# Kernel tuning notes

Measured on AMD Instinct MI355X. Metric: run time of the kernel, lower is better.

## Reference

```python
import jax, jax.numpy as jnp
import numpy as np

DIM = 32      # state dim (enc_shape[0])
LDIM = 256    # latent dim (enc_shape[-1])
N_AUX = LDIM // 2
AUX_H = 128   # aux hidden
ENC_H = 256   # encoder hidden
T = 64        # n_shifts
N = 1024      # batch
DT = 0.01


def setup_inputs() -> dict:
    key = jax.random.key(0)
    ks = jax.random.split(key, 13)
    def w(k, shape, fan):
        return jax.random.normal(k, shape, jnp.float32) / np.sqrt(fan).astype(np.float32)
    return {
        "xs": jax.random.normal(ks[0], (N, T, DIM), jnp.float32),
        # encoder MLP: dim -> 256 -> 256 -> ldim (last layer has no bias)
        "enc_W1": w(ks[1], (DIM, ENC_H), DIM), "enc_b1": w(ks[2], (ENC_H,), ENC_H),
        "enc_W2": w(ks[3], (ENC_H, ENC_H), ENC_H), "enc_b2": w(ks[4], (ENC_H,), ENC_H),
        "enc_W3": w(ks[5], (ENC_H, LDIM), ENC_H),
        # n_aux independent aux MLPs: dim -> 128 -> 128 -> 2 (last no bias), stacked
        "aux_W1": w(ks[6], (N_AUX, DIM, AUX_H), DIM), "aux_b1": w(ks[7], (N_AUX, AUX_H), AUX_H),
        "aux_W2": w(ks[8], (N_AUX, AUX_H, AUX_H), AUX_H), "aux_b2": w(ks[9], (N_AUX, AUX_H), AUX_H),
        "aux_W3": w(ks[10], (N_AUX, AUX_H, 2), AUX_H),
        # C: Linear(ldim, dim, bias=False); stored as [ldim, dim] so x_next = y @ C_W
        "C_W": w(ks[11], (LDIM, DIM), LDIM),
    }


def reference(xs, enc_W1, enc_b1, enc_W2, enc_b2, enc_W3,
              aux_W1, aux_b1, aux_W2, aux_b2, aux_W3, C_W):
    x0 = xs[:, 0, :]                                    # [N, dim]
    # all n_aux tiny MLPs batched via einsum (instead of python loop)
    h = jax.nn.relu(jnp.einsum('nd,kdh->nkh', x0, aux_W1) + aux_b1)
    h = jax.nn.relu(jnp.einsum('nkh,khg->nkg', h, aux_W2) + aux_b2)
    aux = jnp.einsum('nkh,kho->nko', h, aux_W3)          # [N, n_aux, 2] -> (mu, omega)
    scale = jnp.exp(aux[..., 0] * DT)
    cos = jnp.cos(aux[..., 1] * DT) * scale              # [N, n_aux]
    sin = jnp.sin(aux[..., 1] * DT) * scale

    # encoder over all n_shifts timesteps
    e = jax.nn.relu(xs @ enc_W1 + enc_b1)
    e = jax.nn.relu(e @ enc_W2 + enc_b2)
    e = e @ enc_W3                                       # [N, T, ldim]
    y = jnp.concatenate([xs, e], axis=-1)                # [N, T, dim+ldim]

    # Koopman recurrence. The original builds a block-diagonal [ldim, ldim]
    # matrix of 2x2 rotation-scaling blocks (block k acts on latent pair
    # (2k, 2k+1)) and applies it as a row-vector bmm: out = y_row @ K with
    # K_block = [[cos, sin], [-sin, cos]]. We apply the blocks directly.
    y0 = e[:, 0, :].reshape(N, N_AUX, 2)
    def step(carry, _):
        y1, y2 = carry[..., 0], carry[..., 1]
        yn = jnp.stack([y1 * cos - y2 * sin, y1 * sin + y2 * cos], axis=-1)
        return yn, yn
    _, ys = jax.lax.scan(step, y0, None, length=T - 1)   # [T-1, N, n_aux, 2]
    ys = jnp.moveaxis(ys, 0, 1).reshape(N, T - 1, LDIM)  # [N, T-1, ldim]

    y_lat = jnp.concatenate([e[:, :1, :], ys], axis=1)          # [N, T, ldim]
    x_pred = jnp.concatenate([xs[:, :1, :], ys @ C_W], axis=1)  # [N, T, dim]
    y_pred = jnp.concatenate([x_pred, y_lat], axis=-1)          # [N, T, dim+ldim]
    return y, y_pred
```

## Files before the change

### kernel.cpp

```cpp
#include <hip/hip_runtime.h>
#include <math.h>

#define N_SEQ 1024
#define T_SEQ 64
#define DIMX  32
#define LDIM  256
#define NAUX  128
#define AUXH  128
#define ENCH  256
#define OUTC  288
#define DT    0.01f

typedef short bf16x8 __attribute__((ext_vector_type(8)));
typedef float f32x4  __attribute__((ext_vector_type(4)));

__device__ __forceinline__ unsigned short f2bf(float f) {
    unsigned u = __builtin_bit_cast(unsigned, f);
    unsigned r = u + 0x7fffu + ((u >> 16) & 1u);
    return (unsigned short)(r >> 16);
}
__device__ __forceinline__ float bf2f(unsigned short h) {
    unsigned u = ((unsigned)h) << 16;
    return __builtin_bit_cast(float, u);
}
__device__ __forceinline__ f32x4 mfma16(bf16x8 a, bf16x8 b, f32x4 c) {
    return __builtin_amdgcn_mfma_f32_16x16x32_bf16(a, b, c, 0, 0, 0);
}

#define CV_ENC   139264
#define PREP_CONV_BLOCKS 576
__global__ __launch_bounds__(256) void prep_kernel(
    const float* __restrict__ eW1, const float* __restrict__ eW2,
    const float* __restrict__ eW3, const float* __restrict__ C_W,
    const float* __restrict__ aW1, const float* __restrict__ aW2,
    unsigned short* __restrict__ encw, float* __restrict__ cwt,
    unsigned short* __restrict__ a1h, unsigned short* __restrict__ a1l,
    unsigned short* __restrict__ a2h, unsigned short* __restrict__ a2l)
{
    __shared__ float tile[32][33];
    const int b   = blockIdx.x;
    const int tid = threadIdx.x;

    if (b < PREP_CONV_BLOCKS) {
        const int idx = b * 256 + tid;
        if (idx < 8192) {
            int c = idx >> 5, k = idx & 31;
            encw[idx] = f2bf(eW1[k * ENCH + c]);
        } else if (idx < 8192 + 65536) {
            int t = idx - 8192; int c = t >> 8, k = t & 255;
            encw[idx] = f2bf(eW2[k * ENCH + c]);
        } else if (idx < CV_ENC) {
            int t = idx - (8192 + 65536); int c = t >> 8, k = t & 255;
            encw[idx] = f2bf(eW3[k * LDIM + c]);
        } else if (idx < CV_ENC + 8192) {
            int t = idx - CV_ENC; int d = t >> 8, l = t & 255;
            cwt[t] = C_W[l * DIMX + d];
        }
        return;
    }

    const int bb0 = b - PREP_CONV_BLOCKS;
    const float* src; unsigned short *dh, *dl; int R, j0, r0;
    if (bb0 < 512) {
        int k = bb0 >> 2; j0 = (bb0 & 3) * 32; r0 = 0; R = 32;
        src = aW1 + (size_t)k * 4096;
        dh = a1h + (size_t)k * 4096; dl = a1l + (size_t)k * 4096;
    } else {
        int bb = bb0 - 512;
        int k = bb >> 4; j0 = ((bb >> 2) & 3) * 32; r0 = (bb & 3) * 32; R = 128;
        src = aW2 + (size_t)k * 16384;
        dh = a2h + (size_t)k * 16384; dl = a2l + (size_t)k * 16384;
    }

    for (int i = tid; i < 1024; i += 256) {
        int rr = i >> 5, jj = i & 31;
        tile[rr][jj] = src[(r0 + rr) * 128 + j0 + jj];
    }
    __syncthreads();
    for (int i = tid; i < 1024; i += 256) {
        int jj = i >> 5, rr = i & 31;
        float w = tile[rr][jj];
        unsigned short hi = f2bf(w);
        int off = (j0 + jj) * R + r0 + rr;
        dh[off] = hi;
        dl[off] = f2bf(w - bf2f(hi));
    }
}

__global__ __launch_bounds__(256) void auxm_kernel(
    const float* __restrict__ xs,
    const unsigned short* __restrict__ W1h, const unsigned short* __restrict__ W1l,
    const float* __restrict__ b1,
    const unsigned short* __restrict__ W2h, const unsigned short* __restrict__ W2l,
    const float* __restrict__ b2,
    const float* __restrict__ W3,
    float* __restrict__ a_ws, float* __restrict__ th_ws)
{
    const int k   = blockIdx.x >> 4;
    const int n0  = (blockIdx.x & 15) << 6;
    const int tid = threadIdx.x;
    const int wv  = tid >> 6;
    const int ln  = tid & 63;
    const int lr  = ln & 15;
    const int g   = ln >> 4;
    const int cb  = wv * 32;

    __shared__ unsigned short x0h[64][40];
    __shared__ unsigned short x0l[64][40];
    __shared__ unsigned short h1h[64][136];
    __shared__ unsigned short h1l[64][136];
    __shared__ float          p3[256];

    for (int i = tid; i < 512; i += 256) {
        int r = i >> 3, qd = i & 7;
        float4 v = *(const float4*)&xs[(size_t)(n0 + r) * (T_SEQ * DIMX) + qd * 4];
        short4 hs, ls;
        float vv[4] = {v.x, v.y, v.z, v.w};
        short* hp = (short*)&hs; short* lp = (short*)&ls;
        #pragma unroll
        for (int u = 0; u < 4; ++u) {
            unsigned short hi = f2bf(vv[u]);
            hp[u] = (short)hi;
            lp[u] = (short)f2bf(vv[u] - bf2f(hi));
        }
        *(short4*)&x0h[r][qd * 4] = hs;
        *(short4*)&x0l[r][qd * 4] = ls;
    }
    __syncthreads();

    {
        const unsigned short* W1hk = W1h + (size_t)k * 4096;
        const unsigned short* W1lk = W1l + (size_t)k * 4096;
        bf16x8 bh[2], bl[2];
        #pragma unroll
        for (int ct = 0; ct < 2; ++ct) {
            int off = (cb + ct * 16 + lr) * 32 + g * 8;
            bh[ct] = *(const bf16x8*)&W1hk[off];
            bl[ct] = *(const bf16x8*)&W1lk[off];
        }
        f32x4 acc[4][2];
        #pragma unroll
        for (int rt = 0; rt < 4; ++rt) {
            bf16x8 ah = *(const bf16x8*)&x0h[rt * 16 + lr][g * 8];
            bf16x8 al = *(const bf16x8*)&x0l[rt * 16 + lr][g * 8];
            #pragma unroll
            for (int ct = 0; ct < 2; ++ct) {
                f32x4 z = {0.f, 0.f, 0.f, 0.f};
                z = mfma16(ah, bl[ct], z);
                z = mfma16(al, bh[ct], z);
                acc[rt][ct] = mfma16(ah, bh[ct], z);
            }
        }
        #pragma unroll
        for (int ct = 0; ct < 2; ++ct) {
            const int col = cb + ct * 16 + lr;
            const float bb = b1[k * 128 + col];
            #pragma unroll
            for (int rt = 0; rt < 4; ++rt)
                #pragma unroll
                for (int i = 0; i < 4; ++i) {
                    float h = fmaxf(acc[rt][ct][i] + bb, 0.f);
                    unsigned short hi = f2bf(h);
                    int row = rt * 16 + g * 4 + i;
                    h1h[row][col] = hi;
                    h1l[row][col] = f2bf(h - bf2f(hi));
                }
        }
    }
    __syncthreads();

    {
        const unsigned short* W2hk = W2h + (size_t)k * 16384;
        const unsigned short* W2lk = W2l + (size_t)k * 16384;
        f32x4 acc[4][2];
        #pragma unroll
        for (int rt = 0; rt < 4; ++rt)
            #pragma unroll
            for (int ct = 0; ct < 2; ++ct) acc[rt][ct] = (f32x4){0.f,0.f,0.f,0.f};

        #pragma unroll
        for (int kk = 0; kk < 4; ++kk) {
            bf16x8 bh[2], bl[2], ah[4], al[4];
            #pragma unroll
            for (int ct = 0; ct < 2; ++ct) {
                int off = (cb + ct * 16 + lr) * 128 + kk * 32 + g * 8;
                bh[ct] = *(const bf16x8*)&W2hk[off];
                bl[ct] = *(const bf16x8*)&W2lk[off];
            }
            #pragma unroll
            for (int rt = 0; rt < 4; ++rt) {
                ah[rt] = *(const bf16x8*)&h1h[rt * 16 + lr][kk * 32 + g * 8];
                al[rt] = *(const bf16x8*)&h1l[rt * 16 + lr][kk * 32 + g * 8];
            }
            #pragma unroll
            for (int rt = 0; rt < 4; ++rt)
                #pragma unroll
                for (int ct = 0; ct < 2; ++ct) {
                    f32x4 z = acc[rt][ct];
                    z = mfma16(ah[rt], bl[ct], z);
                    z = mfma16(al[rt], bh[ct], z);
                    acc[rt][ct] = mfma16(ah[rt], bh[ct], z);
                }
        }
        __syncthreads();
        #pragma unroll
        for (int ct = 0; ct < 2; ++ct) {
            const int col = cb + ct * 16 + lr;
            const float bb = b2[k * 128 + col];
            #pragma unroll
            for (int rt = 0; rt < 4; ++rt)
                #pragma unroll
                for (int i = 0; i < 4; ++i) {
                    float h = fmaxf(acc[rt][ct][i] + bb, 0.f);
                    unsigned short hi = f2bf(h);
                    int row = rt * 16 + g * 4 + i;
                    h1h[row][col] = hi;
                    h1l[row][col] = f2bf(h - bf2f(hi));
                }
        }
    }
    __syncthreads();

    {
        const int hh = tid >> 7, r = tid & 127, n = r >> 1, o = r & 1;
        const float* W3k = W3 + (size_t)k * (AUXH * 2);
        float s = 0.f;
        #pragma unroll
        for (int h8 = hh * 64; h8 < hh * 64 + 64; h8 += 8) {
            bf16x8 vh = *(const bf16x8*)&h1h[n][h8];
            bf16x8 vl = *(const bf16x8*)&h1l[n][h8];
            #pragma unroll
            for (int u = 0; u < 8; ++u) {
                float hv = bf2f((unsigned short)vh[u]) + bf2f((unsigned short)vl[u]);
                s += hv * W3k[(h8 + u) * 2 + o];
            }
        }
        p3[tid] = s;
    }
    __syncthreads();
    if (tid < 128) {
        const int n = tid >> 1, o = tid & 1;
        float v = (p3[tid] + p3[tid + 128]) * DT;
        float* dst = o ? th_ws : a_ws;
        dst[(size_t)(n0 + n) * NAUX + k] = v;
    }
}

__global__ __launch_bounds__(256) void encm_kernel(
    const float* __restrict__ xs,
    const unsigned short* __restrict__ W1T, const float* __restrict__ b1,
    const unsigned short* __restrict__ W2T, const float* __restrict__ b2,
    const unsigned short* __restrict__ W3T,
    float* __restrict__ y)
{
    __shared__ float          Xf[64 * 36];
    __shared__ unsigned short Hs[64 * 264];

    const int tid = threadIdx.x;
    const int wv  = tid >> 6;
    const int ln  = tid & 63;
    const int lr  = ln & 15;
    const int g   = ln >> 4;
    const int cb  = wv * 64;
    const size_t row0 = (size_t)blockIdx.x * 64;

    {
        const float4* src = (const float4*)(xs + row0 * DIMX);
        for (int i = tid; i < 512; i += 256) {
            int r = i >> 3, q = i & 7;
            *(float4*)&Xf[r * 36 + q * 4] = src[i];
        }
    }
    __syncthreads();

    {
        f32x4 acc[4][4];
        bf16x8 bfr[4], afr[4];
        #pragma unroll
        for (int ct = 0; ct < 4; ++ct)
            bfr[ct] = *(const bf16x8*)&W1T[(cb + ct * 16 + lr) * 32 + g * 8];
        #pragma unroll
        for (int rt = 0; rt < 4; ++rt) {
            const float* xp = &Xf[(rt * 16 + lr) * 36 + g * 8];
            float4 u = *(const float4*)xp;
            float4 v = *(const float4*)(xp + 4);
            bf16x8 t;
            t[0]=(short)f2bf(u.x); t[1]=(short)f2bf(u.y); t[2]=(short)f2bf(u.z); t[3]=(short)f2bf(u.w);
            t[4]=(short)f2bf(v.x); t[5]=(short)f2bf(v.y); t[6]=(short)f2bf(v.z); t[7]=(short)f2bf(v.w);
            afr[rt] = t;
        }
        #pragma unroll
        for (int rt = 0; rt < 4; ++rt)
            #pragma unroll
            for (int ct = 0; ct < 4; ++ct) {
                f32x4 z = {0.f, 0.f, 0.f, 0.f};
                acc[rt][ct] = mfma16(afr[rt], bfr[ct], z);
            }
        #pragma unroll
        for (int ct = 0; ct < 4; ++ct) {
            const float bb = b1[cb + ct * 16 + lr];
            #pragma unroll
            for (int rt = 0; rt < 4; ++rt)
                #pragma unroll
                for (int i = 0; i < 4; ++i) {
                    float h = fmaxf(acc[rt][ct][i] + bb, 0.f);
                    Hs[(rt * 16 + g * 4 + i) * 264 + cb + ct * 16 + lr] = f2bf(h);
                }
        }
    }
    __syncthreads();

    int wrow[4], hoff[4];
    #pragma unroll
    for (int ct = 0; ct < 4; ++ct) wrow[ct] = (cb + ct * 16 + lr) * 256 + g * 8;
    #pragma unroll
    for (int rt = 0; rt < 4; ++rt) hoff[rt] = (rt * 16 + lr) * 264 + g * 8;

    {
        f32x4 acc[4][4];
        #pragma unroll
        for (int rt = 0; rt < 4; ++rt)
            #pragma unroll
            for (int ct = 0; ct < 4; ++ct) acc[rt][ct] = (f32x4){0.f,0.f,0.f,0.f};
        #pragma unroll 2
        for (int kk = 0; kk < 8; ++kk) {
            bf16x8 bfr[4], afr[4];
            #pragma unroll
            for (int ct = 0; ct < 4; ++ct)
                bfr[ct] = *(const bf16x8*)&W2T[wrow[ct] + kk * 32];
            #pragma unroll
            for (int rt = 0; rt < 4; ++rt)
                afr[rt] = *(const bf16x8*)&Hs[hoff[rt] + kk * 32];
            #pragma unroll
            for (int rt = 0; rt < 4; ++rt)
                #pragma unroll
                for (int ct = 0; ct < 4; ++ct)
                    acc[rt][ct] = mfma16(afr[rt], bfr[ct], acc[rt][ct]);
        }
        __syncthreads();
        #pragma unroll
        for (int ct = 0; ct < 4; ++ct) {
            const float bb = b2[cb + ct * 16 + lr];
            #pragma unroll
            for (int rt = 0; rt < 4; ++rt)
                #pragma unroll
                for (int i = 0; i < 4; ++i) {
                    float h = fmaxf(acc[rt][ct][i] + bb, 0.f);
                    Hs[(rt * 16 + g * 4 + i) * 264 + cb + ct * 16 + lr] = f2bf(h);
                }
        }
    }
    __syncthreads();

    {
        f32x4 acc[4][4];
        #pragma unroll
        for (int rt = 0; rt < 4; ++rt)
            #pragma unroll
            for (int ct = 0; ct < 4; ++ct) acc[rt][ct] = (f32x4){0.f,0.f,0.f,0.f};
        #pragma unroll 2
        for (int kk = 0; kk < 8; ++kk) {
            bf16x8 bfr[4], afr[4];
            #pragma unroll
            for (int ct = 0; ct < 4; ++ct)
                bfr[ct] = *(const bf16x8*)&W3T[wrow[ct] + kk * 32];
            #pragma unroll
            for (int rt = 0; rt < 4; ++rt)
                afr[rt] = *(const bf16x8*)&Hs[hoff[rt] + kk * 32];
            #pragma unroll
            for (int rt = 0; rt < 4; ++rt)
                #pragma unroll
                for (int ct = 0; ct < 4; ++ct)
                    acc[rt][ct] = mfma16(afr[rt], bfr[ct], acc[rt][ct]);
        }
        #pragma unroll
        for (int ct = 0; ct < 4; ++ct) {
            const int c3 = cb + ct * 16 + lr;
            #pragma unroll
            for (int rt = 0; rt < 4; ++rt)
                #pragma unroll
                for (int i = 0; i < 4; ++i)
                    y[(row0 + rt * 16 + g * 4 + i) * OUTC + DIMX + c3] = acc[rt][ct][i];
        }
    }

    for (int i = tid; i < 512; i += 256) {
        int r = i >> 3, q = i & 7;
        *(float4*)&y[(row0 + r) * OUTC + q * 4] = *(const float4*)&Xf[r * 36 + q * 4];
    }
}

__global__ __launch_bounds__(256) void enc0_kernel(
    const float* __restrict__ xs,
    const float* __restrict__ W1, const float* __restrict__ b1,
    const float* __restrict__ W2, const float* __restrict__ b2,
    const float* __restrict__ W3,
    float* __restrict__ y)
{
    __shared__ float Xs[4 * 32];
    __shared__ float Hsf[4 * 256];
    const int tid = threadIdx.x;
    const int c   = tid;
    const int n0  = blockIdx.x * 4;

    if (tid < 32) {
        int r = tid >> 3, q = tid & 7;
        *(float4*)&Xs[r * 32 + q * 4] =
            *(const float4*)&xs[(size_t)(n0 + r) * (T_SEQ * DIMX) + q * 4];
    }
    __syncthreads();

    float acc[4];
    {
        float w[32];
        #pragma unroll
        for (int d = 0; d < 32; ++d) w[d] = W1[d * ENCH + c];
        const float bb = b1[c];
        #pragma unroll
        for (int r = 0; r < 4; ++r) {
            float a = bb;
            #pragma unroll
            for (int d4 = 0; d4 < 8; ++d4) {
                float4 xv = *(const float4*)&Xs[r * 32 + d4 * 4];
                a += xv.x * w[d4*4] + xv.y * w[d4*4+1] + xv.z * w[d4*4+2] + xv.w * w[d4*4+3];
            }
            acc[r] = a;
        }
        #pragma unroll
        for (int r = 0; r < 4; ++r) Hsf[r * 256 + c] = fmaxf(acc[r], 0.f);
    }
    __syncthreads();
    {
        const float bb = b2[c];
        #pragma unroll
        for (int r = 0; r < 4; ++r) acc[r] = bb;
        for (int hc = 0; hc < 8; ++hc) {
            float w[32];
            #pragma unroll
            for (int i = 0; i < 32; ++i) w[i] = W2[(hc * 32 + i) * ENCH + c];
            #pragma unroll
            for (int r = 0; r < 4; ++r) {
                float a = acc[r];
                #pragma unroll
                for (int h4 = 0; h4 < 8; ++h4) {
                    float4 hv = *(const float4*)&Hsf[r * 256 + hc * 32 + h4 * 4];
                    a += hv.x * w[h4*4] + hv.y * w[h4*4+1] + hv.z * w[h4*4+2] + hv.w * w[h4*4+3];
                }
                acc[r] = a;
            }
        }
        __syncthreads();
        #pragma unroll
        for (int r = 0; r < 4; ++r) Hsf[r * 256 + c] = fmaxf(acc[r], 0.f);
    }
    __syncthreads();
    {
        #pragma unroll
        for (int r = 0; r < 4; ++r) acc[r] = 0.f;
        for (int hc = 0; hc < 8; ++hc) {
            float w[32];
            #pragma unroll
            for (int i = 0; i < 32; ++i) w[i] = W3[(hc * 32 + i) * LDIM + c];
            #pragma unroll
            for (int r = 0; r < 4; ++r) {
                float a = acc[r];
                #pragma unroll
                for (int h4 = 0; h4 < 8; ++h4) {
                    float4 hv = *(const float4*)&Hsf[r * 256 + hc * 32 + h4 * 4];
                    a += hv.x * w[h4*4] + hv.y * w[h4*4+1] + hv.z * w[h4*4+2] + hv.w * w[h4*4+3];
                }
                acc[r] = a;
            }
        }
    }
    #pragma unroll
    for (int r = 0; r < 4; ++r)
        y[((size_t)(n0 + r) * T_SEQ) * OUTC + DIMX + c] = acc[r];
}

__global__ __launch_bounds__(256) void scan3_kernel(
    const float* __restrict__ xs,
    const float* __restrict__ a_ws, const float* __restrict__ th_ws,
    const float* __restrict__ cwt,
    const float* __restrict__ y,
    float* __restrict__ yp)
{
    __shared__ float ys_lds[16][256];

    const int n = blockIdx.x >> 2;
    const int q = blockIdx.x & 3;
    const int e = threadIdx.x;
    const int k = e >> 1;

    const float* yrow0 = y + (size_t)n * T_SEQ * OUTC + DIMX;
    float2 y0 = *(const float2*)&yrow0[e & ~1];
    const float a  = a_ws [n * NAUX + k];
    const float th = th_ws[n * NAUX + k];

    const float m = expf(a);
    float ss, cc; sincosf(th, &ss, &cc);
    const float zr = m * cc, zi = m * ss;

    float pr = zr, pi = zi;
    #pragma unroll
    for (int s2 = 0; s2 < 4; ++s2) {
        float nr = pr * pr - pi * pi;
        pi = 2.f * pr * pi; pr = nr;
    }
    float wr = 1.f, wi = 0.f;
    for (int j = 0; j < q; ++j) {
        float nr = wr * pr - wi * pi;
        wi = wr * pi + wi * pr; wr = nr;
    }

    const bool imag = e & 1;
    float* ypn = yp + (size_t)n * T_SEQ * OUTC;

    #pragma unroll 4
    for (int tl = 0; tl < 16; ++tl) {
        const int t = q * 16 + tl;
        float val = imag ? (y0.x * wi + y0.y * wr)
                         : (y0.x * wr - y0.y * wi);
        ypn[(size_t)t * OUTC + DIMX + e] = val;
        ys_lds[tl][(e + ((tl >> 1) & 7) * 4) & 255] = val;
        float nwr = wr * zr - wi * zi;
        wi = wr * zi + wi * zr;
        wr = nwr;
    }
    __syncthreads();

    const int d  = e >> 3;
    const int tg = e & 7;
    const float* cwd = cwt + d * 256;
    const int rot = tg * 4;

    #pragma unroll
    for (int s = 0; s < 2; ++s) {
        const int tl = tg * 2 + s;
        const int t  = q * 16 + tl;
        float o;
        if (t == 0) {
            o = xs[(size_t)n * T_SEQ * DIMX + d];
        } else {
            float sum = 0.f;
            #pragma unroll 8
            for (int l = 0; l < 256; l += 4) {
                const int c0 = (l + rot) & 255;
                float4 yv = *(const float4*)&ys_lds[tl][c0];
                float4 wv = *(const float4*)&cwd[l];
                sum += yv.x * wv.x + yv.y * wv.y + yv.z * wv.z + yv.w * wv.w;
            }
            o = sum;
        }
        ypn[(size_t)t * OUTC + d] = o;
    }
}

extern "C" void kernel_launch(void* const* d_in, const int* in_sizes, int n_in,
                              void* d_out, int out_size, void* d_ws, size_t ws_size,
                              hipStream_t stream)
{
    const float* xs   = (const float*)d_in[0];
    const float* eW1  = (const float*)d_in[1];
    const float* eb1  = (const float*)d_in[2];
    const float* eW2  = (const float*)d_in[3];
    const float* eb2  = (const float*)d_in[4];
    const float* eW3  = (const float*)d_in[5];
    const float* aW1  = (const float*)d_in[6];
    const float* ab1  = (const float*)d_in[7];
    const float* aW2  = (const float*)d_in[8];
    const float* ab2  = (const float*)d_in[9];
    const float* aW3  = (const float*)d_in[10];
    const float* C_W  = (const float*)d_in[11];

    float* y  = (float*)d_out;
    float* yp = y + (size_t)N_SEQ * T_SEQ * OUTC;

    float* a_ws  = (float*)d_ws;
    float* th_ws = a_ws + (size_t)N_SEQ * NAUX;
    unsigned short* encw = (unsigned short*)(th_ws + (size_t)N_SEQ * NAUX);
    unsigned short* W1T = encw;
    unsigned short* W2T = encw + 8192;
    unsigned short* W3T = encw + 8192 + 65536;
    unsigned short* a1h = encw + CV_ENC;
    unsigned short* a1l = a1h + 524288;
    unsigned short* a2h = a1l + 524288;
    unsigned short* a2l = a2h + 2097152;
    float* cwt = (float*)(a2l + 2097152);

    prep_kernel<<<PREP_CONV_BLOCKS + 2560, 256, 0, stream>>>(
        eW1, eW2, eW3, C_W, aW1, aW2, encw, cwt, a1h, a1l, a2h, a2l);
    auxm_kernel <<<128 * 16, 256, 0, stream>>>(
        xs, a1h, a1l, ab1, a2h, a2l, ab2, aW3, a_ws, th_ws);
    encm_kernel <<<N_SEQ * T_SEQ / 64, 256, 0, stream>>>(xs, W1T, eb1, W2T, eb2, W3T, y);
    enc0_kernel <<<N_SEQ / 4, 256, 0, stream>>>(xs, eW1, eb1, eW2, eb2, eW3, y);
    scan3_kernel<<<N_SEQ * 4, 256, 0, stream>>>(xs, a_ws, th_ws, cwt, y, yp);
}
```

Measured before the change: 190.9 us.

## Merge aux and encoder kernels into one launch, fold enc0 into prep

The aux-MLP and encoder-MFMA kernels are combined into a single main_kernel whose block index picks the role, so both workloads share one launch and can overlap on the GPU. The fp32 t=0 encoder pass is moved into extra blocks of the prep kernel, and the encoder's output write now skips row t=0 so that row keeps the fp32 result. The scan's C projection computes two timesteps together so each weight load is reused. This cuts two launches and the idle tails between them, in exchange for a larger shared-memory footprint and more branching per block.

```diff
diff --git a/kernel.cpp b/kernel.cpp
--- a/kernel.cpp
+++ b/kernel.cpp
@@ -13,13 +13,14 @@
 
 typedef short bf16x8 __attribute__((ext_vector_type(8)));
 typedef float f32x4  __attribute__((ext_vector_type(4)));
-
-__device__ __forceinline__ unsigned short f2bf(float f) {
+typedef unsigned short ush;
+
+__device__ __forceinline__ ush f2bf(float f) {
     unsigned u = __builtin_bit_cast(unsigned, f);
     unsigned r = u + 0x7fffu + ((u >> 16) & 1u);
-    return (unsigned short)(r >> 16);
+    return (ush)(r >> 16);
 }
-__device__ __forceinline__ float bf2f(unsigned short h) {
+__device__ __forceinline__ float bf2f(ush h) {
     unsigned u = ((unsigned)h) << 16;
     return __builtin_bit_cast(float, u);
 }
@@ -29,15 +30,20 @@
 
 #define CV_ENC   139264
 #define PREP_CONV_BLOCKS 576
+#define PREP_TR_BLOCKS   2560
+#define PREP_ENC0_BLOCKS 256
 __global__ __launch_bounds__(256) void prep_kernel(
-    const float* __restrict__ eW1, const float* __restrict__ eW2,
+    const float* __restrict__ eW1, const float* __restrict__ eb1,
+    const float* __restrict__ eW2, const float* __restrict__ eb2,
     const float* __restrict__ eW3, const float* __restrict__ C_W,
     const float* __restrict__ aW1, const float* __restrict__ aW2,
-    unsigned short* __restrict__ encw, float* __restrict__ cwt,
-    unsigned short* __restrict__ a1h, unsigned short* __restrict__ a1l,
-    unsigned short* __restrict__ a2h, unsigned short* __restrict__ a2l)
+    const float* __restrict__ xs,
+    ush* __restrict__ encw, float* __restrict__ cwt,
+    ush* __restrict__ a1h, ush* __restrict__ a1l,
+    ush* __restrict__ a2h, ush* __restrict__ a2l,
+    float* __restrict__ y)
 {
-    __shared__ float tile[32][33];
+    __shared__ float psm[1152];
     const int b   = blockIdx.x;
     const int tid = threadIdx.x;
 
@@ -59,423 +65,433 @@
         return;
     }
 
-    const int bb0 = b - PREP_CONV_BLOCKS;
-    const float* src; unsigned short *dh, *dl; int R, j0, r0;
-    if (bb0 < 512) {
-        int k = bb0 >> 2; j0 = (bb0 & 3) * 32; r0 = 0; R = 32;
-        src = aW1 + (size_t)k * 4096;
-        dh = a1h + (size_t)k * 4096; dl = a1l + (size_t)k * 4096;
-    } else {
-        int bb = bb0 - 512;
-        int k = bb >> 4; j0 = ((bb >> 2) & 3) * 32; r0 = (bb & 3) * 32; R = 128;
-        src = aW2 + (size_t)k * 16384;
-        dh = a2h + (size_t)k * 16384; dl = a2l + (size_t)k * 16384;
-    }
-
-    for (int i = tid; i < 1024; i += 256) {
-        int rr = i >> 5, jj = i & 31;
-        tile[rr][jj] = src[(r0 + rr) * 128 + j0 + jj];
-    }
-    __syncthreads();
-    for (int i = tid; i < 1024; i += 256) {
-        int jj = i >> 5, rr = i & 31;
-        float w = tile[rr][jj];
-        unsigned short hi = f2bf(w);
-        int off = (j0 + jj) * R + r0 + rr;
-        dh[off] = hi;
-        dl[off] = f2bf(w - bf2f(hi));
+    if (b < PREP_CONV_BLOCKS + PREP_TR_BLOCKS) {
+        float (*tile)[33] = (float(*)[33])psm;
+        const int bb0 = b - PREP_CONV_BLOCKS;
+        const float* src; ush *dh, *dl; int R, j0, r0;
+        if (bb0 < 512) {
+            int k = bb0 >> 2; j0 = (bb0 & 3) * 32; r0 = 0; R = 32;
+            src = aW1 + (size_t)k * 4096;
+            dh = a1h + (size_t)k * 4096; dl = a1l + (size_t)k * 4096;
+        } else {
+            int bb = bb0 - 512;
+            int k = bb >> 4; j0 = ((bb >> 2) & 3) * 32; r0 = (bb & 3) * 32; R = 128;
+            src = aW2 + (size_t)k * 16384;
+            dh = a2h + (size_t)k * 16384; dl = a2l + (size_t)k * 16384;
+        }
+        for (int i = tid; i < 1024; i += 256) {
+            int rr = i >> 5, jj = i & 31;
+            tile[rr][jj] = src[(r0 + rr) * 128 + j0 + jj];
+        }
+        __syncthreads();
+        for (int i = tid; i < 1024; i += 256) {
+            int jj = i >> 5, rr = i & 31;
+            float w = tile[rr][jj];
+            ush hi = f2bf(w);
+            int off = (j0 + jj) * R + r0 + rr;
+            dh[off] = hi;
+            dl[off] = f2bf(w - bf2f(hi));
+        }
+        return;
+    }
+
+    {
+        float* Xs  = psm;
+        float* Hsf = psm + 128;
+        const int c  = tid;
+        const int n0 = (b - PREP_CONV_BLOCKS - PREP_TR_BLOCKS) * 4;
+
+        if (tid < 32) {
+            int r = tid >> 3, q = tid & 7;
+            *(float4*)&Xs[r * 32 + q * 4] =
+                *(const float4*)&xs[(size_t)(n0 + r) * (T_SEQ * DIMX) + q * 4];
+        }
+        __syncthreads();
+
+        float acc[4];
+        {
+            float w[32];
+            #pragma unroll
+            for (int d = 0; d < 32; ++d) w[d] = eW1[d * ENCH + c];
+            const float bb = eb1[c];
+            #pragma unroll
+            for (int r = 0; r < 4; ++r) {
+                float a = bb;
+                #pragma unroll
+                for (int d4 = 0; d4 < 8; ++d4) {
+                    float4 xv = *(const float4*)&Xs[r * 32 + d4 * 4];
+                    a += xv.x * w[d4*4] + xv.y * w[d4*4+1] + xv.z * w[d4*4+2] + xv.w * w[d4*4+3];
+                }
+                acc[r] = a;
+            }
+            #pragma unroll
+            for (int r = 0; r < 4; ++r) Hsf[r * 256 + c] = fmaxf(acc[r], 0.f);
+        }
+        __syncthreads();
+        {
+            const float bb = eb2[c];
+            #pragma unroll
+            for (int r = 0; r < 4; ++r) acc[r] = bb;
+            for (int hc = 0; hc < 8; ++hc) {
+                float w[32];
+                #pragma unroll
+                for (int i = 0; i < 32; ++i) w[i] = eW2[(hc * 32 + i) * ENCH + c];
+                #pragma unroll
+                for (int r = 0; r < 4; ++r) {
+                    float a = acc[r];
+                    #pragma unroll
+                    for (int h4 = 0; h4 < 8; ++h4) {
+                        float4 hv = *(const float4*)&Hsf[r * 256 + hc * 32 + h4 * 4];
+                        a += hv.x * w[h4*4] + hv.y * w[h4*4+1] + hv.z * w[h4*4+2] + hv.w * w[h4*4+3];
+                    }
+                    acc[r] = a;
+                }
+            }
+            __syncthreads();
+            #pragma unroll
+            for (int r = 0; r < 4; ++r) Hsf[r * 256 + c] = fmaxf(acc[r], 0.f);
+        }
+        __syncthreads();
+        {
+            #pragma unroll
+            for (int r = 0; r < 4; ++r) acc[r] = 0.f;
+            for (int hc = 0; hc < 8; ++hc) {
+                float w[32];
+                #pragma unroll
+                for (int i = 0; i < 32; ++i) w[i] = eW3[(hc * 32 + i) * LDIM + c];
+                #pragma unroll
+                for (int r = 0; r < 4; ++r) {
+                    float a = acc[r];
+                    #pragma unroll
+                    for (int h4 = 0; h4 < 8; ++h4) {
+                        float4 hv = *(const float4*)&Hsf[r * 256 + hc * 32 + h4 * 4];
+                        a += hv.x * w[h4*4] + hv.y * w[h4*4+1] + hv.z * w[h4*4+2] + hv.w * w[h4*4+3];
+                    }
+                    acc[r] = a;
+                }
+            }
+        }
+        #pragma unroll
+        for (int r = 0; r < 4; ++r)
+            y[((size_t)(n0 + r) * T_SEQ) * OUTC + DIMX + c] = acc[r];
     }
 }
 
-__global__ __launch_bounds__(256) void auxm_kernel(
+__global__ __launch_bounds__(256) void main_kernel(
     const float* __restrict__ xs,
-    const unsigned short* __restrict__ W1h, const unsigned short* __restrict__ W1l,
-    const float* __restrict__ b1,
-    const unsigned short* __restrict__ W2h, const unsigned short* __restrict__ W2l,
-    const float* __restrict__ b2,
-    const float* __restrict__ W3,
-    float* __restrict__ a_ws, float* __restrict__ th_ws)
+    const ush* __restrict__ W1h, const ush* __restrict__ W1l,
+    const float* __restrict__ ab1,
+    const ush* __restrict__ W2h, const ush* __restrict__ W2l,
+    const float* __restrict__ ab2,
+    const float* __restrict__ aW3,
+    float* __restrict__ a_ws, float* __restrict__ th_ws,
+    const ush* __restrict__ W1T, const float* __restrict__ eb1,
+    const ush* __restrict__ W2T, const float* __restrict__ eb2,
+    const ush* __restrict__ W3T,
+    float* __restrict__ y)
 {
-    const int k   = blockIdx.x >> 4;
-    const int n0  = (blockIdx.x & 15) << 6;
+    __shared__ __align__(16) char smem[46080];
     const int tid = threadIdx.x;
     const int wv  = tid >> 6;
     const int ln  = tid & 63;
     const int lr  = ln & 15;
     const int g   = ln >> 4;
-    const int cb  = wv * 32;
-
-    __shared__ unsigned short x0h[64][40];
-    __shared__ unsigned short x0l[64][40];
-    __shared__ unsigned short h1h[64][136];
-    __shared__ unsigned short h1l[64][136];
-    __shared__ float          p3[256];
-
-    for (int i = tid; i < 512; i += 256) {
-        int r = i >> 3, qd = i & 7;
-        float4 v = *(const float4*)&xs[(size_t)(n0 + r) * (T_SEQ * DIMX) + qd * 4];
-        short4 hs, ls;
-        float vv[4] = {v.x, v.y, v.z, v.w};
-        short* hp = (short*)&hs; short* lp = (short*)&ls;
+
+    if (blockIdx.x < 2048) {
+        ush (*x0h)[40]  = (ush(*)[40]) (smem);
+        ush (*x0l)[40]  = (ush(*)[40]) (smem + 5120);
+        ush (*h1h)[136] = (ush(*)[136])(smem + 10240);
+        ush (*h1l)[136] = (ush(*)[136])(smem + 27648);
+        float* p3       = (float*)     (smem + 45056);
+
+        const int k   = blockIdx.x >> 4;
+        const int n0  = (blockIdx.x & 15) << 6;
+        const int cb  = wv * 32;
+
+        for (int i = tid; i < 512; i += 256) {
+            int r = i >> 3, qd = i & 7;
+            float4 v = *(const float4*)&xs[(size_t)(n0 + r) * (T_SEQ * DIMX) + qd * 4];
+            short4 hs, ls;
+            float vv[4] = {v.x, v.y, v.z, v.w};
+            short* hp = (short*)&hs; short* lp = (short*)&ls;
+            #pragma unroll
+            for (int u = 0; u < 4; ++u) {
+                ush hi = f2bf(vv[u]);
+                hp[u] = (short)hi;
+                lp[u] = (short)f2bf(vv[u] - bf2f(hi));
+            }
+            *(short4*)&x0h[r][qd * 4] = hs;
+            *(short4*)&x0l[r][qd * 4] = ls;
+        }
+        __syncthreads();
+
+        {
+            const ush* W1hk = W1h + (size_t)k * 4096;
+            const ush* W1lk = W1l + (size_t)k * 4096;
+            bf16x8 bh[2], bl[2];
+            #pragma unroll
+            for (int ct = 0; ct < 2; ++ct) {
+                int off = (cb + ct * 16 + lr) * 32 + g * 8;
+                bh[ct] = *(const bf16x8*)&W1hk[off];
+                bl[ct] = *(const bf16x8*)&W1lk[off];
+            }
+            f32x4 acc[4][2];
+            #pragma unroll
+            for (int rt = 0; rt < 4; ++rt) {
+                bf16x8 ah = *(const bf16x8*)&x0h[rt * 16 + lr][g * 8];
+                bf16x8 al = *(const bf16x8*)&x0l[rt * 16 + lr][g * 8];
+                #pragma unroll
+                for (int ct = 0; ct < 2; ++ct) {
+                    f32x4 z = {0.f, 0.f, 0.f, 0.f};
+                    z = mfma16(ah, bl[ct], z);
+                    z = mfma16(al, bh[ct], z);
+                    acc[rt][ct] = mfma16(ah, bh[ct], z);
+                }
+            }
+            #pragma unroll
+            for (int ct = 0; ct < 2; ++ct) {
+                const int col = cb + ct * 16 + lr;
+                const float bb = ab1[k * 128 + col];
+                #pragma unroll
+                for (int rt = 0; rt < 4; ++rt)
+                    #pragma unroll
+                    for (int i = 0; i < 4; ++i) {
+                        float h = fmaxf(acc[rt][ct][i] + bb, 0.f);
+                        ush hi = f2bf(h);
+                        int row = rt * 16 + g * 4 + i;
+                        h1h[row][col] = hi;
+                        h1l[row][col] = f2bf(h - bf2f(hi));
+                    }
+            }
+        }
+        __syncthreads();
+
+        {
+            const ush* W2hk = W2h + (size_t)k * 16384;
+            const ush* W2lk = W2l + (size_t)k * 16384;
+            f32x4 acc[4][2];
+            #pragma unroll
+            for (int rt = 0; rt < 4; ++rt)
+                #pragma unroll
+                for (int ct = 0; ct < 2; ++ct) acc[rt][ct] = (f32x4){0.f,0.f,0.f,0.f};
+
+            #pragma unroll
+            for (int kk = 0; kk < 4; ++kk) {
+                bf16x8 bh[2], bl[2], ah[4], al[4];
+                #pragma unroll
+                for (int ct = 0; ct < 2; ++ct) {
+                    int off = (cb + ct * 16 + lr) * 128 + kk * 32 + g * 8;
+                    bh[ct] = *(const bf16x8*)&W2hk[off];
+                    bl[ct] = *(const bf16x8*)&W2lk[off];
+                }
+                #pragma unroll
+                for (int rt = 0; rt < 4; ++rt) {
+                    ah[rt] = *(const bf16x8*)&h1h[rt * 16 + lr][kk * 32 + g * 8];
+                    al[rt] = *(const bf16x8*)&h1l[rt * 16 + lr][kk * 32 + g * 8];
+                }
+                #pragma unroll
+                for (int rt = 0; rt < 4; ++rt)
+                    #pragma unroll
+                    for (int ct = 0; ct < 2; ++ct) {
+                        f32x4 z = acc[rt][ct];
+                        z = mfma16(ah[rt], bl[ct], z);
+                        z = mfma16(al[rt], bh[ct], z);
+                        acc[rt][ct] = mfma16(ah[rt], bh[ct], z);
+                    }
+            }
+            __syncthreads();
+            #pragma unroll
+            for (int ct = 0; ct < 2; ++ct) {
+                const int col = cb + ct * 16 + lr;
+                const float bb = ab2[k * 128 + col];
+                #pragma unroll
+                for (int rt = 0; rt < 4; ++rt)
+                    #pragma unroll
+                    for (int i = 0; i < 4; ++i) {
+                        float h = fmaxf(acc[rt][ct][i] + bb, 0.f);
+                        ush hi = f2bf(h);
+                        int row = rt * 16 + g * 4 + i;
+                        h1h[row][col] = hi;
+                        h1l[row][col] = f2bf(h - bf2f(hi));
+                    }
+            }
+        }
+        __syncthreads();
+
+        {
+            const int hh = tid >> 7, r = tid & 127, n = r >> 1, o = r & 1;
+            const float* W3k = aW3 + (size_t)k * (AUXH * 2);
+            float s = 0.f;
+            #pragma unroll
+            for (int h8 = hh * 64; h8 < hh * 64 + 64; h8 += 8) {
+                bf16x8 vh = *(const bf16x8*)&h1h[n][h8];
+                bf16x8 vl = *(const bf16x8*)&h1l[n][h8];
+                #pragma unroll
+                for (int u = 0; u < 8; ++u) {
+                    float hv = bf2f((ush)vh[u]) + bf2f((ush)vl[u]);
+                    s += hv * W3k[(h8 + u) * 2 + o];
+                }
+            }
+            p3[tid] = s;
+        }
+        __syncthreads();
+        if (tid < 128) {
+            const int n = tid >> 1, o = tid & 1;
+            float v = (p3[tid] + p3[tid + 128]) * DT;
+            float* dst = o ? th_ws : a_ws;
+            dst[(size_t)(n0 + n) * NAUX + k] = v;
+        }
+        return;
+    }
+
+    {
+        float* Xf = (float*)smem;
+        ush*   Hs = (ush*)(smem + 9216);
+
+        const int cb  = wv * 64;
+        const size_t row0 = (size_t)(blockIdx.x - 2048) * 64;
+
+        {
+            const float4* src = (const float4*)(xs + row0 * DIMX);
+            for (int i = tid; i < 512; i += 256) {
+                int r = i >> 3, q = i & 7;
+                *(float4*)&Xf[r * 36 + q * 4] = src[i];
+            }
+        }
+        __syncthreads();
+
+        {
+            f32x4 acc[4][4];
+            bf16x8 bfr[4], afr[4];
+            #pragma unroll
+            for (int ct = 0; ct < 4; ++ct)
+                bfr[ct] = *(const bf16x8*)&W1T[(cb + ct * 16 + lr) * 32 + g * 8];
+            #pragma unroll
+            for (int rt = 0; rt < 4; ++rt) {
+                const float* xp = &Xf[(rt * 16 + lr) * 36 + g * 8];
+                float4 u = *(const float4*)xp;
+                float4 v = *(const float4*)(xp + 4);
+                bf16x8 t;
+                t[0]=(short)f2bf(u.x); t[1]=(short)f2bf(u.y); t[2]=(short)f2bf(u.z); t[3]=(short)f2bf(u.w);
+                t[4]=(short)f2bf(v.x); t[5]=(short)f2bf(v.y); t[6]=(short)f2bf(v.z); t[7]=(short)f2bf(v.w);
+                afr[rt] = t;
+            }
+            #pragma unroll
+            for (int rt = 0; rt < 4; ++rt)
+                #pragma unroll
+                for (int ct = 0; ct < 4; ++ct) {
+                    f32x4 z = {0.f, 0.f, 0.f, 0.f};
+                    acc[rt][ct] = mfma16(afr[rt], bfr[ct], z);
+                }
+            #pragma unroll
+            for (int ct = 0; ct < 4; ++ct) {
+                const float bb = eb1[cb + ct * 16 + lr];
+                #pragma unroll
+                for (int rt = 0; rt < 4; ++rt)
+                    #pragma unroll
+                    for (int i = 0; i < 4; ++i) {
+                        float h = fmaxf(acc[rt][ct][i] + bb, 0.f);
+                        Hs[(rt * 16 + g * 4 + i) * 264 + cb + ct * 16 + lr] = f2bf(h);
+                    }
+            }
+        }
+        __syncthreads();
+
+        int wrow[4], hoff[4];
         #pragma unroll
-        for (int u = 0; u < 4; ++u) {
-            unsigned short hi = f2bf(vv[u]);
-            hp[u] = (short)hi;
-            lp[u] = (short)f2bf(vv[u] - bf2f(hi));
-        }
-        *(short4*)&x0h[r][qd * 4] = hs;
-        *(short4*)&x0l[r][qd * 4] = ls;
-    }
-    __syncthreads();
-
-    {
-        const unsigned short* W1hk = W1h + (size_t)k * 4096;
-        const unsigned short* W1lk = W1l + (size_t)k * 4096;
-        bf16x8 bh[2], bl[2];
+        for (int ct = 0; ct < 4; ++ct) wrow[ct] = (cb + ct * 16 + lr) * 256 + g * 8;
         #pragma unroll
-        for (int ct = 0; ct < 2; ++ct) {
-            int off = (cb + ct * 16 + lr) * 32 + g * 8;
-            bh[ct] = *(const bf16x8*)&W1hk[off];
-            bl[ct] = *(const bf16x8*)&W1lk[off];
-        }
-        f32x4 acc[4][2];
-        #pragma unroll
-        for (int rt = 0; rt < 4; ++rt) {
-            bf16x8 ah = *(const bf16x8*)&x0h[rt * 16 + lr][g * 8];
-            bf16x8 al = *(const bf16x8*)&x0l[rt * 16 + lr][g * 8];
-            #pragma unroll
-            for (int ct = 0; ct < 2; ++ct) {
-                f32x4 z = {0.f, 0.f, 0.f, 0.f};
-                z = mfma16(ah, bl[ct], z);
-                z = mfma16(al, bh[ct], z);
-                acc[rt][ct] = mfma16(ah, bh[ct], z);
-            }
-        }
-        #pragma unroll
-        for (int ct = 0; ct < 2; ++ct) {
-            const int col = cb + ct * 16 + lr;
-            const float bb = b1[k * 128 + col];
+        for (int rt = 0; rt < 4; ++rt) hoff[rt] = (rt * 16 + lr) * 264 + g * 8;
+
+        {
+            f32x4 acc[4][4];
             #pragma unroll
             for (int rt = 0; rt < 4; ++rt)
                 #pragma unroll
-                for (int i = 0; i < 4; ++i) {
-                    float h = fmaxf(acc[rt][ct][i] + bb, 0.f);
-                    unsigned short hi = f2bf(h);
-                    int row = rt * 16 + g * 4 + i;
-                    h1h[row][col] = hi;
-                    h1l[row][col] = f2bf(h - bf2f(hi));
-                }
-        }
-    }
-    __syncthreads();
-
-    {
-        const unsigned short* W2hk = W2h + (size_t)k * 16384;
-        const unsigned short* W2lk = W2l + (size_t)k * 16384;
-        f32x4 acc[4][2];
-        #pragma unroll
-        for (int rt = 0; rt < 4; ++rt)
-            #pragma unroll
-            for (int ct = 0; ct < 2; ++ct) acc[rt][ct] = (f32x4){0.f,0.f,0.f,0.f};
-
-        #pragma unroll
-        for (int kk = 0; kk < 4; ++kk) {
-            bf16x8 bh[2], bl[2], ah[4], al[4];
-            #pragma unroll
-            for (int ct = 0; ct < 2; ++ct) {
-                int off = (cb + ct * 16 + lr) * 128 + kk * 32 + g * 8;
-                bh[ct] = *(const bf16x8*)&W2hk[off];
-                bl[ct] = *(const bf16x8*)&W2lk[off];
-            }
-            #pragma unroll
-            for (int rt = 0; rt < 4; ++rt) {
-                ah[rt] = *(const bf16x8*)&h1h[rt * 16 + lr][kk * 32 + g * 8];
-                al[rt] = *(const bf16x8*)&h1l[rt * 16 + lr][kk * 32 + g * 8];
-            }
+                for (int ct = 0; ct < 4; ++ct) acc[rt][ct] = (f32x4){0.f,0.f,0.f,0.f};
+            #pragma unroll 2
+            for (int kk = 0; kk < 8; ++kk) {
+                bf16x8 bfr[4], afr[4];
+                #pragma unroll
+                for (int ct = 0; ct < 4; ++ct)
+                    bfr[ct] = *(const bf16x8*)&W2T[wrow[ct] + kk * 32];
+                #pragma unroll
+                for (int rt = 0; rt < 4; ++rt)
+                    afr[rt] = *(const bf16x8*)&Hs[hoff[rt] + kk * 32];
+                #pragma unroll
+                for (int rt = 0; rt < 4; ++rt)
+                    #pragma unroll
+                    for (int ct = 0; ct < 4; ++ct)
+                        acc[rt][ct] = mfma16(afr[rt], bfr[ct], acc[rt][ct]);
+            }
+            __syncthreads();
+            #pragma unroll
+            for (int ct = 0; ct < 4; ++ct) {
+                const float bb = eb2[cb + ct * 16 + lr];
+                #pragma unroll
+                for (int rt = 0; rt < 4; ++rt)
+                    #pragma unroll
+                    for (int i = 0; i < 4; ++i) {
+                        float h = fmaxf(acc[rt][ct][i] + bb, 0.f);
+                        Hs[(rt * 16 + g * 4 + i) * 264 + cb + ct * 16 + lr] = f2bf(h);
+                    }
+            }
+        }
+        __syncthreads();
+
+        {
+            f32x4 acc[4][4];
             #pragma unroll
             for (int rt = 0; rt < 4; ++rt)
                 #pragma unroll
-                for (int ct = 0; ct < 2; ++ct) {
-                    f32x4 z = acc[rt][ct];
-                    z = mfma16(ah[rt], bl[ct], z);
-                    z = mfma16(al[rt], bh[ct], z);
-                    acc[rt][ct] = mfma16(ah[rt], bh[ct], z);
-                }
-        }
-        __syncthreads();
-        #pragma unroll
-        for (int ct = 0; ct < 2; ++ct) {
-            const int col = cb + ct * 16 + lr;
-            const float bb = b2[k * 128 + col];
-            #pragma unroll
-            for (int rt = 0; rt < 4; ++rt)
-                #pragma unroll
-                for (int i = 0; i < 4; ++i) {
-                    float h = fmaxf(acc[rt][ct][i] + bb, 0.f);
-                    unsigned short hi = f2bf(h);
-                    int row = rt * 16 + g * 4 + i;
-                    h1h[row][col] = hi;
-                    h1l[row][col] = f2bf(h - bf2f(hi));
-                }
-        }
-    }
-    __syncthreads();
-
-    {
-        const int hh = tid >> 7, r = tid & 127, n = r >> 1, o = r & 1;
-        const float* W3k = W3 + (size_t)k * (AUXH * 2);
-        float s = 0.f;
-        #pragma unroll
-        for (int h8 = hh * 64; h8 < hh * 64 + 64; h8 += 8) {
-            bf16x8 vh = *(const bf16x8*)&h1h[n][h8];
-            bf16x8 vl = *(const bf16x8*)&h1l[n][h8];
-            #pragma unroll
-            for (int u = 0; u < 8; ++u) {
-                float hv = bf2f((unsigned short)vh[u]) + bf2f((unsigned short)vl[u]);
-                s += hv * W3k[(h8 + u) * 2 + o];
-            }
-        }
-        p3[tid] = s;
-    }
-    __syncthreads();
-    if (tid < 128) {
-        const int n = tid >> 1, o = tid & 1;
-        float v = (p3[tid] + p3[tid + 128]) * DT;
-        float* dst = o ? th_ws : a_ws;
-        dst[(size_t)(n0 + n) * NAUX + k] = v;
-    }
-}
-
-__global__ __launch_bounds__(256) void encm_kernel(
-    const float* __restrict__ xs,
-    const unsigned short* __restrict__ W1T, const float* __restrict__ b1,
-    const unsigned short* __restrict__ W2T, const float* __restrict__ b2,
-    const unsigned short* __restrict__ W3T,
-    float* __restrict__ y)
-{
-    __shared__ float          Xf[64 * 36];
-    __shared__ unsigned short Hs[64 * 264];
-
-    const int tid = threadIdx.x;
-    const int wv  = tid >> 6;
-    const int ln  = tid & 63;
-    const int lr  = ln & 15;
-    const int g   = ln >> 4;
-    const int cb  = wv * 64;
-    const size_t row0 = (size_t)blockIdx.x * 64;
-
-    {
-        const float4* src = (const float4*)(xs + row0 * DIMX);
-        for (int i = tid; i < 512; i += 256) {
-            int r = i >> 3, q = i & 7;
-            *(float4*)&Xf[r * 36 + q * 4] = src[i];
-        }
-    }
-    __syncthreads();
-
-    {
-        f32x4 acc[4][4];
-        bf16x8 bfr[4], afr[4];
-        #pragma unroll
-        for (int ct = 0; ct < 4; ++ct)
-            bfr[ct] = *(const bf16x8*)&W1T[(cb + ct * 16 + lr) * 32 + g * 8];
-        #pragma unroll
-        for (int rt = 0; rt < 4; ++rt) {
-            const float* xp = &Xf[(rt * 16 + lr) * 36 + g * 8];
-            float4 u = *(const float4*)xp;
-            float4 v = *(const float4*)(xp + 4);
-            bf16x8 t;
-            t[0]=(short)f2bf(u.x); t[1]=(short)f2bf(u.y); t[2]=(short)f2bf(u.z); t[3]=(short)f2bf(u.w);
-            t[4]=(short)f2bf(v.x); t[5]=(short)f2bf(v.y); t[6]=(short)f2bf(v.z); t[7]=(short)f2bf(v.w);
-            afr[rt] = t;
-        }
-        #pragma unroll
-        for (int rt = 0; rt < 4; ++rt)
-            #pragma unroll
-            for (int ct = 0; ct < 4; ++ct) {
-                f32x4 z = {0.f, 0.f, 0.f, 0.f};
-                acc[rt][ct] = mfma16(afr[rt], bfr[ct], z);
-            }
-        #pragma unroll
-        for (int ct = 0; ct < 4; ++ct) {
-            const float bb = b1[cb + ct * 16 + lr];
-            #pragma unroll
-            for (int rt = 0; rt < 4; ++rt)
-                #pragma unroll
-                for (int i = 0; i < 4; ++i) {
-                    float h = fmaxf(acc[rt][ct][i] + bb, 0.f);
-                    Hs[(rt * 16 + g * 4 + i) * 264 + cb + ct * 16 + lr] = f2bf(h);
-                }
-        }
-    }
-    __syncthreads();
-
-    int wrow[4], hoff[4];
-    #pragma unroll
-    for (int ct = 0; ct < 4; ++ct) wrow[ct] = (cb + ct * 16 + lr) * 256 + g * 8;
-    #pragma unroll
-    for (int rt = 0; rt < 4; ++rt) hoff[rt] = (rt * 16 + lr) * 264 + g * 8;
-
-    {
-        f32x4 acc[4][4];
-        #pragma unroll
-        for (int rt = 0; rt < 4; ++rt)
-            #pragma unroll
-            for (int ct = 0; ct < 4; ++ct) acc[rt][ct] = (f32x4){0.f,0.f,0.f,0.f};
-        #pragma unroll 2
-        for (int kk = 0; kk < 8; ++kk) {
-            bf16x8 bfr[4], afr[4];
-            #pragma unroll
-            for (int ct = 0; ct < 4; ++ct)
-                bfr[ct] = *(const bf16x8*)&W2T[wrow[ct] + kk * 32];
-            #pragma unroll
-            for (int rt = 0; rt < 4; ++rt)
-                afr[rt] = *(const bf16x8*)&Hs[hoff[rt] + kk * 32];
-            #pragma unroll
-            for (int rt = 0; rt < 4; ++rt)
+                for (int ct = 0; ct < 4; ++ct) acc[rt][ct] = (f32x4){0.f,0.f,0.f,0.f};
+            #pragma unroll 2
+            for (int kk = 0; kk < 8; ++kk) {
+                bf16x8 bfr[4], afr[4];
                 #pragma unroll
                 for (int ct = 0; ct < 4; ++ct)
-                    acc[rt][ct] = mfma16(afr[rt], bfr[ct], acc[rt][ct]);
-        }
-        __syncthreads();
-        #pragma unroll
-        for (int ct = 0; ct < 4; ++ct) {
-            const float bb = b2[cb + ct * 16 + lr];
-            #pragma unroll
-            for (int rt = 0; rt < 4; ++rt)
-                #pragma unroll
-                for (int i = 0; i < 4; ++i) {
-                    float h = fmaxf(acc[rt][ct][i] + bb, 0.f);
-                    Hs[(rt * 16 + g * 4 + i) * 264 + cb + ct * 16 + lr] = f2bf(h);
-                }
-        }
-    }
-    __syncthreads();
-
-    {
-        f32x4 acc[4][4];
-        #pragma unroll
-        for (int rt = 0; rt < 4; ++rt)
-            #pragma unroll
-            for (int ct = 0; ct < 4; ++ct) acc[rt][ct] = (f32x4){0.f,0.f,0.f,0.f};
-        #pragma unroll 2
-        for (int kk = 0; kk < 8; ++kk) {
-            bf16x8 bfr[4], afr[4];
-            #pragma unroll
-            for (int ct = 0; ct < 4; ++ct)
-                bfr[ct] = *(const bf16x8*)&W3T[wrow[ct] + kk * 32];
-            #pragma unroll
-            for (int rt = 0; rt < 4; ++rt)
-                afr[rt] = *(const bf16x8*)&Hs[hoff[rt] + kk * 32];
-            #pragma unroll
-            for (int rt = 0; rt < 4; ++rt)
-                #pragma unroll
-                for (int ct = 0; ct < 4; ++ct)
-                    acc[rt][ct] = mfma16(afr[rt], bfr[ct], acc[rt][ct]);
-        }
-        #pragma unroll
-        for (int ct = 0; ct < 4; ++ct) {
-            const int c3 = cb + ct * 16 + lr;
-            #pragma unroll
-            for (int rt = 0; rt < 4; ++rt)
-                #pragma unroll
-                for (int i = 0; i < 4; ++i)
-                    y[(row0 + rt * 16 + g * 4 + i) * OUTC + DIMX + c3] = acc[rt][ct][i];
-        }
-    }
-
-    for (int i = tid; i < 512; i += 256) {
-        int r = i >> 3, q = i & 7;
-        *(float4*)&y[(row0 + r) * OUTC + q * 4] = *(const float4*)&Xf[r * 36 + q * 4];
-    }
-}
-
-__global__ __launch_bounds__(256) void enc0_kernel(
-    const float* __restrict__ xs,
-    const float* __restrict__ W1, const float* __restrict__ b1,
-    const float* __restrict__ W2, const float* __restrict__ b2,
-    const float* __restrict__ W3,
-    float* __restrict__ y)
-{
-    __shared__ float Xs[4 * 32];
-    __shared__ float Hsf[4 * 256];
-    const int tid = threadIdx.x;
-    const int c   = tid;
-    const int n0  = blockIdx.x * 4;
-
-    if (tid < 32) {
-        int r = tid >> 3, q = tid & 7;
-        *(float4*)&Xs[r * 32 + q * 4] =
-            *(const float4*)&xs[(size_t)(n0 + r) * (T_SEQ * DIMX) + q * 4];
-    }
-    __syncthreads();
-
-    float acc[4];
-    {
-        float w[32];
-        #pragma unroll
-        for (int d = 0; d < 32; ++d) w[d] = W1[d * ENCH + c];
-        const float bb = b1[c];
-        #pragma unroll
-        for (int r = 0; r < 4; ++r) {
-            float a = bb;
-            #pragma unroll
-            for (int d4 = 0; d4 < 8; ++d4) {
-                float4 xv = *(const float4*)&Xs[r * 32 + d4 * 4];
-                a += xv.x * w[d4*4] + xv.y * w[d4*4+1] + xv.z * w[d4*4+2] + xv.w * w[d4*4+3];
-            }
-            acc[r] = a;
-        }
-        #pragma unroll
-        for (int r = 0; r < 4; ++r) Hsf[r * 256 + c] = fmaxf(acc[r], 0.f);
-    }
-    __syncthreads();
-    {
-        const float bb = b2[c];
-        #pragma unroll
-        for (int r = 0; r < 4; ++r) acc[r] = bb;
-        for (int hc = 0; hc < 8; ++hc) {
-            float w[32];
-            #pragma unroll
-            for (int i = 0; i < 32; ++i) w[i] = W2[(hc * 32 + i) * ENCH + c];
-            #pragma unroll
-            for (int r = 0; r < 4; ++r) {
-                float a = acc[r];
-                #pragma unroll
-                for (int h4 = 0; h4 < 8; ++h4) {
-                    float4 hv = *(const float4*)&Hsf[r * 256 + hc * 32 + h4 * 4];
-                    a += hv.x * w[h4*4] + hv.y * w[h4*4+1] + hv.z * w[h4*4+2] + hv.w * w[h4*4+3];
-                }
-                acc[r] = a;
-            }
-        }
-        __syncthreads();
-        #pragma unroll
-        for (int r = 0; r < 4; ++r) Hsf[r * 256 + c] = fmaxf(acc[r], 0.f);
-    }
-    __syncthreads();
-    {
-        #pragma unroll
-        for (int r = 0; r < 4; ++r) acc[r] = 0.f;
-        for (int hc = 0; hc < 8; ++hc) {
-            float w[32];
-            #pragma unroll
-            for (int i = 0; i < 32; ++i) w[i] = W3[(hc * 32 + i) * LDIM + c];
-            #pragma unroll
-            for (int r = 0; r < 4; ++r) {
-                float a = acc[r];
-                #pragma unroll
-                for (int h4 = 0; h4 < 8; ++h4) {
-                    float4 hv = *(const float4*)&Hsf[r * 256 + hc * 32 + h4 * 4];
-                    a += hv.x * w[h4*4] + hv.y * w[h4*4+1] + hv.z * w[h4*4+2] + hv.w * w[h4*4+3];
-                }
-                acc[r] = a;
-            }
-        }
-    }
-    #pragma unroll
-    for (int r = 0; r < 4; ++r)
-        y[((size_t)(n0 + r) * T_SEQ) * OUTC + DIMX + c] = acc[r];
+                    bfr[ct] = *(const bf16x8*)&W3T[wrow[ct] + kk * 32];
+                #pragma unroll
+                for (int rt = 0; rt < 4; ++rt)
+                    afr[rt] = *(const bf16x8*)&Hs[hoff[rt] + kk * 32];
+                #pragma unroll
+                for (int rt = 0; rt < 4; ++rt)
+                    #pragma unroll
+                    for (int ct = 0; ct < 4; ++ct)
+                        acc[rt][ct] = mfma16(afr[rt], bfr[ct], acc[rt][ct]);
+            }
+            __syncthreads();
+
+            float* HsF = (float*)Hs;
+            const int r  = tid >> 3;
+            const int ce = tid & 7;
+
+            #pragma unroll
+            for (int p = 0; p < 2; ++p) {
+                #pragma unroll
+                for (int rt = 2 * p; rt < 2 * p + 2; ++rt)
+                    #pragma unroll
+                    for (int ct = 0; ct < 4; ++ct)
+                        #pragma unroll
+                        for (int i = 0; i < 4; ++i)
+                            HsF[((rt - 2 * p) * 16 + g * 4 + i) * 264 + cb + ct * 16 + lr]
+                                = acc[rt][ct][i];
+                __syncthreads();
+                const int rloc = p * 32 + r;
+                float* dstrow = &y[(row0 + rloc) * OUTC];
+                #pragma unroll
+                for (int j = 0; j < 9; ++j) {
+                    int f4 = j * 8 + ce;
+                    float4 v;
+                    if (f4 < 8) v = *(const float4*)&Xf[rloc * 36 + f4 * 4];
+                    else        v = *(const float4*)&HsF[r * 264 + (f4 - 8) * 4];
+                    if (!(rloc == 0 && f4 >= 8))
+                        *(float4*)&dstrow[f4 * 4] = v;
+                }
+                __syncthreads();
+            }
+        }
+    }
 }
 
 __global__ __launch_bounds__(256) void scan3_kernel(
@@ -529,31 +545,27 @@
     }
     __syncthreads();
 
-    const int d  = e >> 3;
-    const int tg = e & 7;
+    const int d   = e >> 3;
+    const int tg  = e & 7;
+    const int tl0 = tg * 2, tl1 = tl0 + 1;
     const float* cwd = cwt + d * 256;
     const int rot = tg * 4;
 
-    #pragma unroll
-    for (int s = 0; s < 2; ++s) {
-        const int tl = tg * 2 + s;
-        const int t  = q * 16 + tl;
-        float o;
-        if (t == 0) {
-            o = xs[(size_t)n * T_SEQ * DIMX + d];
-        } else {
-            float sum = 0.f;
-            #pragma unroll 8
-            for (int l = 0; l < 256; l += 4) {
-                const int c0 = (l + rot) & 255;
-                float4 yv = *(const float4*)&ys_lds[tl][c0];
-                float4 wv = *(const float4*)&cwd[l];
-                sum += yv.x * wv.x + yv.y * wv.y + yv.z * wv.z + yv.w * wv.w;
-            }
-            o = sum;
-        }
-        ypn[(size_t)t * OUTC + d] = o;
-    }
+    float s0 = 0.f, s1 = 0.f;
+    #pragma unroll 8
+    for (int l = 0; l < 256; l += 4) {
+        const int c0 = (l + rot) & 255;
+        float4 wv = *(const float4*)&cwd[l];
+        float4 ya = *(const float4*)&ys_lds[tl0][c0];
+        float4 yb = *(const float4*)&ys_lds[tl1][c0];
+        s0 += ya.x * wv.x + ya.y * wv.y + ya.z * wv.z + ya.w * wv.w;
+        s1 += yb.x * wv.x + yb.y * wv.y + yb.z * wv.z + yb.w * wv.w;
+    }
+    const int t0 = q * 16 + tl0;
+    const int t1 = q * 16 + tl1;
+    float o0 = (t0 == 0) ? xs[(size_t)n * T_SEQ * DIMX + d] : s0;
+    ypn[(size_t)t0 * OUTC + d] = o0;
+    ypn[(size_t)t1 * OUTC + d] = s1;
 }
 
 extern "C" void kernel_launch(void* const* d_in, const int* in_sizes, int n_in,
@@ -578,21 +590,21 @@
 
     float* a_ws  = (float*)d_ws;
     float* th_ws = a_ws + (size_t)N_SEQ * NAUX;
-    unsigned short* encw = (unsigned short*)(th_ws + (size_t)N_SEQ * NAUX);
-    unsigned short* W1T = encw;
-    unsigned short* W2T = encw + 8192;
-    unsigned short* W3T = encw + 8192 + 65536;
-    unsigned short* a1h = encw + CV_ENC;
-    unsigned short* a1l = a1h + 524288;
-    unsigned short* a2h = a1l + 524288;
-    unsigned short* a2l = a2h + 2097152;
+    ush* encw = (ush*)(th_ws + (size_t)N_SEQ * NAUX);
+    ush* W1T = encw;
+    ush* W2T = encw + 8192;
+    ush* W3T = encw + 8192 + 65536;
+    ush* a1h = encw + CV_ENC;
+    ush* a1l = a1h + 524288;
+    ush* a2h = a1l + 524288;
+    ush* a2l = a2h + 2097152;
     float* cwt = (float*)(a2l + 2097152);
 
-    prep_kernel<<<PREP_CONV_BLOCKS + 2560, 256, 0, stream>>>(
-        eW1, eW2, eW3, C_W, aW1, aW2, encw, cwt, a1h, a1l, a2h, a2l);
-    auxm_kernel <<<128 * 16, 256, 0, stream>>>(
-        xs, a1h, a1l, ab1, a2h, a2l, ab2, aW3, a_ws, th_ws);
-    encm_kernel <<<N_SEQ * T_SEQ / 64, 256, 0, stream>>>(xs, W1T, eb1, W2T, eb2, W3T, y);
-    enc0_kernel <<<N_SEQ / 4, 256, 0, stream>>>(xs, eW1, eb1, eW2, eb2, eW3, y);
+    prep_kernel<<<PREP_CONV_BLOCKS + PREP_TR_BLOCKS + PREP_ENC0_BLOCKS, 256, 0, stream>>>(
+        eW1, eb1, eW2, eb2, eW3, C_W, aW1, aW2, xs,
+        encw, cwt, a1h, a1l, a2h, a2l, y);
+    main_kernel<<<3072, 256, 0, stream>>>(
+        xs, a1h, a1l, ab1, a2h, a2l, ab2, aW3, a_ws, th_ws,
+        W1T, eb1, W2T, eb2, W3T, y);
     scan3_kernel<<<N_SEQ * 4, 256, 0, stream>>>(xs, a_ws, th_ws, cwt, y, yp);
 }
```

Measured after the change: 166.3 us. -12.9%, faster.
